# Performance work log

Measured on AMD Instinct MI355X. Metric: run time of the kernel, lower is better.

## Reference

```python
import jax, jax.numpy as jnp
import numpy as np

B, N, M = 4, 1024, 100
NB = 25
NTYPE = 2
TYPES = (1, 8)
FEAT = NB * NTYPE  # 50
H = 100
PI = 3.1415926
RMIN, RMAX = 0.5, 6.0


def setup_inputs() -> dict:
    key = jax.random.key(0)
    ks = jax.random.split(key, 12)
    type_map = jnp.array(TYPES)
    Imagetype = type_map[jax.random.randint(ks[0], (B, N), 0, NTYPE)]
    neighbor_list = jax.random.randint(ks[1], (B, N, M), 0, N + 1)
    rij = jax.random.uniform(ks[2], (B, N, M), minval=0.5, maxval=7.0)
    d = jax.random.normal(ks[3], (B, N, M, 3))
    d = d / jnp.linalg.norm(d, axis=-1, keepdims=True)
    ImagedR = jnp.concatenate([rij[..., None], d * rij[..., None]], axis=-1).astype(jnp.float32)

    def w(k, i, o):
        return (jax.random.normal(k, (NTYPE, i, o)) / np.sqrt(i + o)).astype(jnp.float32)

    def b(k, o):
        return jax.random.normal(k, (NTYPE, o)).astype(jnp.float32)

    return {"Imagetype": Imagetype, "neighbor_list": neighbor_list, "ImagedR": ImagedR,
            "W0": w(ks[4], FEAT, H), "b0": b(ks[5], H),
            "W1": w(ks[6], H, H), "b1": b(ks[7], H),
            "W2": w(ks[8], H, H), "b2": b(ks[9], H),
            "W3": w(ks[10], H, 1), "b3": b(ks[11], 1)}


def _net(x, W0, b0, W1, b1, W2, b2, W3, b3):
    # NET with network_size [50,100,100,100,1], tanh, resnet_dt=False
    h = jnp.tanh(x @ W0 + b0)
    x = h + jnp.concatenate([x, x], axis=-1)  # 50 -> 100 doubling skip
    h = jnp.tanh(x @ W1 + b1); x = h + x
    h = jnp.tanh(x @ W2 + b2); x = h + x
    return x @ W3 + b3


def _body2fun(Imagetype, neighbor_list, ImagedR):
    Bn, Nn, Mn = neighbor_list.shape
    rs = jnp.linspace(RMIN, RMAX, NB)  # [NB]
    r = ImagedR[..., 0]  # [B,N,M]
    rb = jnp.broadcast_to(r[..., None], (Bn, Nn, Mn, NB))

    def fc_fn(rt):
        env = jnp.exp(-(rt - rs) ** 2) * (0.5 * jnp.cos(PI * rt) + 0.5)
        return jnp.where((rt < RMAX) & (rt > 0), env, 0.0)

    # dfc = d(fc)/dr, elementwise, matching torch.autograd.grad with ones
    fc, dfc = jax.jvp(fc_fn, (rb,), (jnp.ones_like(rb),))

    # neighbor_type: 1-indexed lookup with 0 -> padding type 0
    padded = jnp.concatenate([jnp.zeros((Bn, 1), Imagetype.dtype), Imagetype], axis=1)
    nt = jnp.take_along_axis(padded, neighbor_list.reshape(Bn, -1), axis=1).reshape(Bn, Nn, Mn)

    dvec = jnp.where(r[..., None] != 0, ImagedR[..., 1:4] / r[..., None], 0.0)  # [B,N,M,3]

    feats, dfeats = [], []
    for t in TYPES:
        m = (nt == t)[..., None]  # [B,N,M,1]
        fct = jnp.where(m, fc, 0.0)
        dfct = jnp.where(m, dfc, 0.0)
        feats.append(fct.sum(axis=2))  # [B,N,NB]
        dfeats.append(dfct[..., None] * dvec[..., None, :])  # [B,N,M,NB,3]
    feat = jnp.concatenate(feats, axis=-1)  # [B,N,50]
    dfeat = jnp.concatenate(dfeats, axis=3)  # [B,N,M,50,3]
    return feat, dfeat


def reference(Imagetype, neighbor_list, ImagedR, W0, b0, W1, b1, W2, b2, W3, b3):
    Bn, Nn, Mn = neighbor_list.shape
    feat, dfeat = _body2fun(Imagetype, neighbor_list, ImagedR)

    type_arr = jnp.array(TYPES)
    mask = (Imagetype[None] == type_arr[:, None, None])[..., None]  # [T,B,N,1]

    def ei_fn(f):
        e = jax.vmap(_net, in_axes=(None, 0, 0, 0, 0, 0, 0, 0, 0))(
            f, W0, b0, W1, b1, W2, b2, W3, b3)  # [T,B,N,1]
        return jnp.sum(jnp.where(mask, e, 0.0), axis=0)  # [B,N,1]

    Ei = ei_fn(feat)
    Etot = jnp.sum(Ei, axis=1)  # [B,1]

    # dE/dfeat of total energy (grad_outputs = ones on Etot)
    dE = jax.grad(lambda f: jnp.sum(ei_fn(f)))(feat)  # [B,N,50]

    dE_Rid = jnp.einsum('bnf,bnmfc->bnmc', dE, dfeat)  # [B,N,M,3]
    Force = -dE_Rid.sum(axis=2)  # [B,N,3]

    # scatter-add of neighbor contributions: segment 0 is padding
    seg = jax.vmap(lambda v, i: jax.ops.segment_sum(v, i, num_segments=Nn + 1))(
        dE_Rid.reshape(Bn, -1, 3), neighbor_list.reshape(Bn, -1))  # [B,N+1,3]
    Force = Force + seg[:, 1:, :]
    return Etot, Ei, Force
```

## Files before the change

kernel.cpp:

```cpp
#include <hip/hip_runtime.h>

#define Bn   4
#define Nn   1024
#define Mn   100
#define NB   25
#define FEAT 50
#define PIc  3.1415926f
#define RSTEP (5.5f / 24.0f)

#define ATB  16
#define NATOMS (Bn * Nn)
#define ORDER_LEN (NATOMS + ATB)
#define MLP_BLOCKS (ORDER_LEN / ATB)
#define TYW  122880
#define PREP_BLKS 341

#define GPB  64
#define CPG  16
#define FTHREADS 512

typedef __attribute__((ext_vector_type(8))) short bf16x8;
typedef __attribute__((ext_vector_type(4))) float f32x4;

union U16x8 { unsigned short u[8]; bf16x8 v; uint4 q; };

__device__ __forceinline__ unsigned short f2bh(float x) {
    union { float f; unsigned u; } v; v.f = x;
    unsigned r = v.u + 0x7fffu + ((v.u >> 16) & 1u);
    return (unsigned short)(r >> 16);
}
__device__ __forceinline__ float bh2f(unsigned short h) {
    union { unsigned u; float f; } v; v.u = ((unsigned)h) << 16; return v.f;
}
__device__ __forceinline__ float fast_tanh(float x) {
    float ax = fabsf(x);
    float t  = __expf(-2.0f * ax);
    float r  = (1.0f - t) * __builtin_amdgcn_rcpf(1.0f + t);
    return copysignf(r, x);
}


__global__ __launch_bounds__(256) void stage1_kernel(
    const int* __restrict__ itype, const int* __restrict__ nlist,
    const float* __restrict__ dR,
    const float* __restrict__ W0, const float* __restrict__ W1,
    const float* __restrict__ W2,
    int* __restrict__ order, unsigned short* __restrict__ wsu,
    float* __restrict__ featp)
{
    const int blk = blockIdx.x;
    const int t = threadIdx.x;

    __shared__ float tile[64][65];
    __shared__ int scan[256];
    __shared__ float4 rc4[50];
    __shared__ float fpartial[64];

    if (blk < 20) {
        int ty = blk / 10, m = blk - ty * 10;
        int mat, jt, kt;
        if (m < 2)      { mat = 0; jt = m;            kt = 0; }
        else if (m < 6) { mat = 1; jt = (m - 2) >> 1; kt = (m - 2) & 1; }
        else            { mat = 2; jt = (m - 6) >> 1; kt = (m - 6) & 1; }
        const float* src = (mat == 0) ? W0 + ty * 5000
                          : (mat == 1) ? W1 + ty * 10000 : W2 + ty * 10000;
        const int Krows = (mat == 0) ? 50 : 100;
        const int Ck    = (mat == 0) ? 64 : 128;
        const int dH = ty * TYW + ((mat == 0) ? 0 : (mat == 1) ? 16384 : 49152);
        const int dL = dH + ((mat == 0) ? 8192 : 16384);
        const int j0 = jt * 64, k0 = kt * 64;
        const int rr0 = t >> 6, l = t & 63;
        #pragma unroll
        for (int i = 0; i < 16; ++i) {
            int rr = rr0 + 4 * i;
            int k = k0 + rr, j = j0 + l;
            tile[rr][l] = (k < Krows && j < 100) ? src[k * 100 + j] : 0.0f;
        }
        __syncthreads();
        #pragma unroll
        for (int i = 0; i < 16; ++i) {
            int jj = rr0 + 4 * i;
            float v = tile[l][jj];
            unsigned short h = f2bh(v);
            wsu[dH + (j0 + jj) * Ck + k0 + l] = h;
            wsu[dL + (j0 + jj) * Ck + k0 + l] = f2bh(v - bh2f(h));
        }
        return;
    }
    if (blk < 340) {
        int e = (blk - 20) * 256 + t;
        int ty = e / 40960;
        int r  = e - ty * 40960;
        float v = 0.0f; int dst;
        if (r < 16384) {
            int i = r >> 7, j = r & 127;
            if (i < 100 && j < 100) v = W2[ty * 10000 + i * 100 + j];
            dst = ty * TYW + 81920 + r;
        } else if (r < 32768) {
            int r2 = r - 16384; int i = r2 >> 7, j = r2 & 127;
            if (i < 100 && j < 100) v = W1[ty * 10000 + i * 100 + j];
            dst = ty * TYW + 98304 + r2;
        } else {
            int r2 = r - 32768; int f = r2 >> 7, j = r2 & 127;
            if (f < 50 && j < 100) v = W0[ty * 5000 + f * 100 + j];
            dst = ty * TYW + 114688 + r2;
        }
        wsu[dst] = f2bh(v);
        return;
    }
    if (blk == 340) {
        for (int i = t; i < ORDER_LEN; i += 256) order[i] = -1;
        int tyv[16]; int c0 = 0;
        #pragma unroll
        for (int k = 0; k < 16; ++k) {
            int tt = (itype[t * 16 + k] == 8) ? 1 : 0;
            tyv[k] = tt; c0 += 1 - tt;
        }
        scan[t] = c0;
        __syncthreads();
        for (int off = 1; off < 256; off <<= 1) {
            int v = scan[t];
            int add = (t >= off) ? scan[t - off] : 0;
            __syncthreads();
            scan[t] = v + add;
            __syncthreads();
        }
        int total0 = scan[255];
        int ex0 = scan[t] - c0;
        int ex1 = 16 * t - ex0;
        int pad0 = (total0 + (ATB - 1)) & ~(ATB - 1);
        int p0 = ex0, p1 = pad0 + ex1;
        #pragma unroll
        for (int k = 0; k < 16; ++k) {
            int idx = t * 16 + k;
            if (tyv[k] == 0) order[p0++] = idx; else order[p1++] = idx;
        }
        return;
    }

    const int atom = blk - PREP_BLKS;
    const int b = atom >> 10;

    if (t < Mn) {
        float4 qv = ((const float4*)dR)[(size_t)atom * Mn + t];
        float r = qv.x;
        int v = nlist[(size_t)atom * Mn + t];
        float cws = 0.0f;
        if (v > 0 && r > 0.0f && r < 6.0f) {
            float cw = 0.5f * __cosf(PIc * r) + 0.5f;
            cws = (itype[b * Nn + (v - 1)] == 8) ? -cw : cw;
        }
        ((float2*)rc4)[t] = make_float2(r, cws);
    }
    __syncthreads();

    float acc = 0.0f;
    if (t < 128) {
        const int w = t >> 6, l = t & 63;
        const int tt = l / NB;
        const float rk = 0.5f + (l - tt * NB) * RSTEP;
        #pragma unroll
        for (int i = 0; i < 25; ++i) {
            float4 pr = rc4[w * 25 + i];
            float d0 = pr.x - rk, d1 = pr.z - rk;
            float c0 = tt ? fmaxf(-pr.y, 0.0f) : fmaxf(pr.y, 0.0f);
            float c1 = tt ? fmaxf(-pr.w, 0.0f) : fmaxf(pr.w, 0.0f);
            acc += __expf(-d0 * d0) * c0 + __expf(-d1 * d1) * c1;
        }
        if (w == 1) fpartial[l] = acc;
    }
    __syncthreads();
    if (t < 64)
        featp[(size_t)atom * 64 + t] = (t < FEAT) ? (acc + fpartial[t]) : 0.0f;
}

#define ISSUE(RH, RL, OFFU, OFFL, RW, NKT, HASLO, COND)                       \
    if (COND) {                                                               \
        int jj_ = c + 16 * w;                                                 \
        _Pragma("unroll")                                                     \
        for (int kt = 0; kt < (NKT); ++kt) {                                  \
            int boff_ = jj_ * (RW) + kt * 32 + q * 8;                         \
            RH[kt] = *(const bf16x8*)(wb + (OFFU) + boff_);                   \
            if (HASLO) RL[kt] = *(const bf16x8*)(wb + (OFFL) + boff_);        \
        }                                                                     \
    }

#define GEMM_R(ABUF, RH, RL, NKT, HASLO)                                      \
    {                                                                         \
        acc = (f32x4){0,0,0,0}; accl = (f32x4){0,0,0,0};                      \
        _Pragma("unroll")                                                     \
        for (int kt = 0; kt < (NKT); ++kt) {                                  \
            int gk = kt * 4 + q;                                              \
            bf16x8 af = *(const bf16x8*)&aA[ABUF][(c << 7) | ((gk ^ (c & 7)) << 3)]; \
            acc = __builtin_amdgcn_mfma_f32_16x16x32_bf16(af, RH[kt], acc, 0, 0, 0); \
            if (HASLO) accl = __builtin_amdgcn_mfma_f32_16x16x32_bf16(af, RL[kt], accl, 0, 0, 0); \
        }                                                                     \
    }

#define WRACT(BUF, J, A, X)                                                   \
    aA[BUF][((A) << 7) | ((((J) >> 3) ^ ((A) & 7)) << 3) | ((J) & 7)] = f2bh(X)

__global__ __launch_bounds__(512) void mlp_kernel(
    const float* __restrict__ featp, const int* __restrict__ itype,
    const int* __restrict__ order, const unsigned short* __restrict__ wsu,
    const float* __restrict__ B0, const float* __restrict__ B1,
    const float* __restrict__ B2, const float* __restrict__ W3,
    const float* __restrict__ B3,
    float* __restrict__ Ei, float* __restrict__ dE)
{
    const int t = threadIdx.x;
    const int w = t >> 6;
    const int lane = t & 63;
    const int c = lane & 15, q = lane >> 4;

    __shared__ unsigned short aA[2][2048];
    __shared__ float fshf[16][52];
    __shared__ float dx1s[16][112];
    __shared__ float biasS[4][128];
    __shared__ float eip[8][16];
    __shared__ int aid[16];

    if (t < 16) aid[t] = order[blockIdx.x * ATB + t];
    __syncthreads();
    int first = -1;
    #pragma unroll
    for (int a = 0; a < ATB; ++a) { int v = aid[a]; if (first < 0 && v >= 0) first = v; }
    if (first < 0) return;
    const int ty = (itype[first] == 8) ? 1 : 0;
    const unsigned short* wb = wsu + (size_t)ty * TYW;

    bf16x8 bh0[4], bl0[4], bh1[4], bl1[4];
    f32x4 acc, accl;
    float xr[4], h0r[4], h1r[4], h2r[4], dxr[4];

    ISSUE(bh0, bl0, 0, 8192, 64, 2, 1, true);
    if (t < 128) {
        const int srow = t >> 3, sg = t & 7;
        int v = aid[srow];
        float4 fa = {0,0,0,0}, fb = {0,0,0,0};
        if (v >= 0) {
            const float4* fp = (const float4*)(featp + (size_t)v * 64 + sg * 8);
            fa = fp[0]; fb = fp[1];
        }
        U16x8 pk;
        pk.u[0]=f2bh(fa.x); pk.u[1]=f2bh(fa.y); pk.u[2]=f2bh(fa.z); pk.u[3]=f2bh(fa.w);
        pk.u[4]=f2bh(fb.x); pk.u[5]=f2bh(fb.y); pk.u[6]=f2bh(fb.z); pk.u[7]=f2bh(fb.w);
        *(uint4*)&aA[0][(srow << 7) | ((sg ^ (srow & 7)) << 3)] = pk.q;
        int cbase = sg * 8;
        if (cbase < 52) {
            float vals[8] = {fa.x,fa.y,fa.z,fa.w,fb.x,fb.y,fb.z,fb.w};
            #pragma unroll
            for (int j7 = 0; j7 < 8; ++j7)
                if (cbase + j7 < 52) fshf[srow][cbase + j7] = vals[j7];
        }
    }
    if (t < 512) {
        int row = t >> 7, col = t & 127;
        const float* s = (row == 0) ? B0 : (row == 1) ? B1 : (row == 2) ? B2 : W3;
        biasS[row][col] = (col < 100) ? s[ty * 100 + col] : 0.0f;
    }
    __syncthreads();

    ISSUE(bh1, bl1, 16384, 32768, 128, 4, 1, true);
    GEMM_R(0, bh0, bl0, 2, 1);
    {
        int j = c + 16 * w;
        float bj = biasS[0][j];
        #pragma unroll
        for (int r = 0; r < 4; ++r) {
            int a = q * 4 + r;
            float z = acc[r] + accl[r] + bj;
            float h = 0.f, x = 0.f;
            if (j < 100) { h = fast_tanh(z); x = h + fshf[a][(j < 50) ? j : j - 50]; }
            h0r[r] = h; xr[r] = x;
            WRACT(1, j, a, x);
        }
    }
    __syncthreads();

    ISSUE(bh0, bl0, 49152, 65536, 128, 4, 1, true);
    GEMM_R(1, bh1, bl1, 4, 1);
    {
        int j = c + 16 * w;
        float bj = biasS[1][j];
        #pragma unroll
        for (int r = 0; r < 4; ++r) {
            int a = q * 4 + r;
            float z = acc[r] + accl[r] + bj;
            float h = (j < 100) ? fast_tanh(z) : 0.f;
            float x = (j < 100) ? (h + xr[r]) : 0.f;
            h1r[r] = h; xr[r] = x;
            WRACT(0, j, a, x);
        }
    }
    __syncthreads();

    ISSUE(bh1, bl1, 81920, 0, 128, 4, 0, true);
    GEMM_R(0, bh0, bl0, 4, 1);
    {
        int j = c + 16 * w;
        float bj = biasS[2][j];
        float wv = biasS[3][j];
        float p4v[4];
        #pragma unroll
        for (int r = 0; r < 4; ++r) {
            float z = acc[r] + accl[r] + bj;
            float h = (j < 100) ? fast_tanh(z) : 0.f;
            h2r[r] = h;
            xr[r] = (j < 100) ? (h + xr[r]) : 0.f;
            p4v[r] = xr[r] * wv;
        }
        #pragma unroll
        for (int off = 1; off < 16; off <<= 1) {
            #pragma unroll
            for (int r = 0; r < 4; ++r) p4v[r] += __shfl_xor(p4v[r], off);
        }
        if (c == 0) {
            #pragma unroll
            for (int r = 0; r < 4; ++r) eip[w][q * 4 + r] = p4v[r];
        }
        #pragma unroll
        for (int r = 0; r < 4; ++r) {
            int a = q * 4 + r;
            float d = wv * (1.0f - h2r[r] * h2r[r]);
            WRACT(1, j, a, d);
        }
    }
    __syncthreads();
    if (t < 16) {
        int v = aid[t];
        if (v >= 0) {
            float e = B3[ty];
            #pragma unroll
            for (int ww = 0; ww < 8; ++ww) e += eip[ww][t];
            Ei[v] = e;
        }
    }

    ISSUE(bh0, bl0, 98304, 0, 128, 4, 0, true);
    GEMM_R(1, bh1, bl1, 4, 0);
    {
        int i = c + 16 * w;
        float w3i = biasS[3][i];
        #pragma unroll
        for (int r = 0; r < 4; ++r) {
            int a = q * 4 + r;
            float dx2 = acc[r] + w3i;
            dxr[r] = dx2;
            float d = dx2 * (1.0f - h1r[r] * h1r[r]);
            WRACT(0, i, a, d);
        }
    }
    __syncthreads();

    ISSUE(bh1, bl1, 114688, 0, 128, 4, 0, (w < 4));
    GEMM_R(0, bh0, bl0, 4, 0);
    {
        int i = c + 16 * w;
        #pragma unroll
        for (int r = 0; r < 4; ++r) {
            int a = q * 4 + r;
            float dx1 = dxr[r] + acc[r];
            if (i < 112) dx1s[a][i] = dx1;
            float d = dx1 * (1.0f - h0r[r] * h0r[r]);
            WRACT(1, i, a, d);
        }
    }
    __syncthreads();

    if (w < 4) {
        GEMM_R(1, bh1, bl1, 4, 0);
        int f = c + 16 * w;
        if (f < 50) {
            #pragma unroll
            for (int r = 0; r < 4; ++r) {
                int a = q * 4 + r;
                int v = aid[a];
                if (v >= 0) dE[(size_t)v * FEAT + f] = acc[r] + dx1s[a][f] + dx1s[a][f + 50];
            }
        }
    }
}

__global__ __launch_bounds__(FTHREADS) void force_kernel(
    const int* __restrict__ itype, const int* __restrict__ nlist,
    const float* __restrict__ dR, const float* __restrict__ dE,
    float* __restrict__ partial)
{
    const int blk = blockIdx.x;
    const int b = blk / GPB;
    const int g = blk - b * GPB;
    const int t = threadIdx.x;
    const int w = t >> 6, lane = t & 63;

    __shared__ float acc[(Nn + 1) * 3];
    __shared__ float desh[CPG][FEAT];

    for (int idx = t; idx < (Nn + 1) * 3; idx += FTHREADS) acc[idx] = 0.0f;
    for (int idx = t; idx < CPG * FEAT; idx += FTHREADS)
        ((float*)desh)[idx] = dE[((size_t)(b * Nn) + g * CPG) * FEAT + idx];
    __syncthreads();

    for (int cc = w; cc < CPG; cc += 8) {
        const int n = g * CPG + cc;
        const size_t pairbase = (size_t)(b * Nn + n) * Mn;

        const int m1 = lane + 64;
        float4 qv0 = ((const float4*)dR)[pairbase + lane];
        int    v0  = nlist[pairbase + lane];
        float4 qv1 = make_float4(0.f, 0.f, 0.f, 0.f);
        int    v1  = 0;
        if (m1 < Mn) {
            qv1 = ((const float4*)dR)[pairbase + m1];
            v1  = nlist[pairbase + m1];
        }

        float cfx = 0.f, cfy = 0.f, cfz = 0.f;
        #pragma unroll
        for (int mi = 0; mi < 2; ++mi) {
            float4 qv = mi ? qv1 : qv0;
            int v = mi ? v1 : v0;
            if (v > 0) {
                float r = qv.x;
                if (r > 0.0f && r < 6.0f) {
                    int tt = (itype[b * Nn + v - 1] == 8) ? 1 : 0;
                    float cw  = 0.5f * __cosf(PIc * r) + 0.5f;
                    float dcw = -0.5f * PIc * __sinf(PIc * r);
                    float s = 0.0f;
                    const float* de = &desh[cc][tt * NB];
                    #pragma unroll
                    for (int k = 0; k < NB; ++k) {
                        float d = r - (0.5f + k * RSTEP);
                        float e = __expf(-d * d);
                        s += de[k] * e * __builtin_fmaf(-2.0f * cw, d, dcw);
                    }
                    float inv = 1.0f / r;
                    float fx = s * qv.y * inv, fy = s * qv.z * inv, fz = s * qv.w * inv;
                    atomicAdd(&acc[v * 3 + 0], fx);
                    atomicAdd(&acc[v * 3 + 1], fy);
                    atomicAdd(&acc[v * 3 + 2], fz);
                    cfx += fx; cfy += fy; cfz += fz;
                }
            }
        }
        #pragma unroll
        for (int off = 32; off > 0; off >>= 1) {
            cfx += __shfl_xor(cfx, off);
            cfy += __shfl_xor(cfy, off);
            cfz += __shfl_xor(cfz, off);
        }
        if (lane == 0) {
            atomicAdd(&acc[(n + 1) * 3 + 0], -cfx);
            atomicAdd(&acc[(n + 1) * 3 + 1], -cfy);
            atomicAdd(&acc[(n + 1) * 3 + 2], -cfz);
        }
    }
    __syncthreads();

    float* pout = partial + (size_t)blk * ((Nn + 1) * 3);
    for (int idx = t; idx < (Nn + 1) * 3; idx += FTHREADS) pout[idx] = acc[idx];
}

__global__ __launch_bounds__(256) void freduce_kernel(
    const float* __restrict__ partial, const float* __restrict__ Ei,
    float* __restrict__ Force, float* __restrict__ Etot)
{
    if (blockIdx.x == 48) {
        const int t = threadIdx.x;
        __shared__ float red[256];
        for (int b = 0; b < Bn; ++b) {
            float s = 0.0f;
            for (int i = t; i < Nn; i += 256) s += Ei[b * Nn + i];
            red[t] = s;
            __syncthreads();
            for (int st = 128; st > 0; st >>= 1) {
                if (t < st) red[t] += red[t + st];
                __syncthreads();
            }
            if (t == 0) Etot[b] = red[0];
            __syncthreads();
        }
        return;
    }
    int idx = blockIdx.x * 256 + threadIdx.x;
    if (idx >= Bn * Nn * 3) return;
    int b = idx / (Nn * 3);
    int r = idx - b * (Nn * 3);
    int i = r / 3, ch = r - i * 3;
    float s = 0.0f;
    for (int g = 0; g < GPB; ++g)
        s += partial[((size_t)(b * GPB + g)) * ((Nn + 1) * 3) + (size_t)(i + 1) * 3 + ch];
    Force[idx] = s;
}

extern "C" void kernel_launch(void* const* d_in, const int* in_sizes, int n_in,
                              void* d_out, int out_size, void* d_ws, size_t ws_size,
                              hipStream_t stream)
{
    const int*   itype = (const int*)d_in[0];
    const int*   nlist = (const int*)d_in[1];
    const float* dR    = (const float*)d_in[2];
    const float* W0 = (const float*)d_in[3];  const float* B0 = (const float*)d_in[4];
    const float* W1 = (const float*)d_in[5];  const float* B1 = (const float*)d_in[6];
    const float* W2 = (const float*)d_in[7];  const float* B2 = (const float*)d_in[8];
    const float* W3 = (const float*)d_in[9];  const float* B3 = (const float*)d_in[10];

    float* out   = (float*)d_out;
    float* Etot  = out;
    float* Ei    = out + Bn;
    float* Force = out + Bn + Bn * Nn;

    float* featp   = (float*)d_ws;
    float* dEp     = featp + (size_t)NATOMS * 64;
    float* partial = dEp + (size_t)NATOMS * FEAT;
    int*   order   = (int*)(partial + (size_t)Bn * GPB * (Nn + 1) * 3);
    unsigned short* wsu = (unsigned short*)(order + ORDER_LEN);

    stage1_kernel <<<PREP_BLKS + NATOMS, 256, 0, stream>>>(itype, nlist, dR,
                                                           W0, W1, W2,
                                                           order, wsu, featp);
    mlp_kernel    <<<MLP_BLOCKS, 512, 0, stream>>>(featp, itype, order, wsu,
                                                   B0, B1, B2, W3, B3, Ei, dEp);
    force_kernel  <<<Bn * GPB, FTHREADS, 0, stream>>>(itype, nlist, dR, dEp, partial);
    freduce_kernel<<<49, 256, 0, stream>>>(partial, Ei, Force, Etot);
}
```

Measured before the change: 51.63 us.

## Fuse MLP and force kernels with per-batch type-sorted atom ordering

Merges the MLP kernel and the force scatter kernel into one kernel. Each block runs the MLP for 16 same-type atoms of a single batch, keeps dE in LDS, and accumulates force contributions into a per-block shared accumulator that is written out as a partial. The type ordering is now computed per batch so every block stays inside one batch, and Etot is accumulated with atomics instead of a separate reduction block. This removes one kernel launch and the global round trip of dE. The cost is a larger LDS footprint per block, 260 blocks instead of 257, and float atomics making Etot order-nondeterministic.

New measurement: 52.67 us. 1.02x slower.

```diff
diff --git a/kernel.cpp b/kernel.cpp
--- a/kernel.cpp
+++ b/kernel.cpp
@@ -10,14 +10,12 @@
 
 #define ATB  16
 #define NATOMS (Bn * Nn)
-#define ORDER_LEN (NATOMS + ATB)
-#define MLP_BLOCKS (ORDER_LEN / ATB)
+#define NGPB  65
+#define OBATCH (NGPB * ATB)
+#define MF_BLOCKS (Bn * NGPB)
 #define TYW  122880
 #define PREP_BLKS 341
-
-#define GPB  64
-#define CPG  16
-#define FTHREADS 512
+#define PSTRIDE ((Nn + 1) * 3)
 
 typedef __attribute__((ext_vector_type(8))) short bf16x8;
 typedef __attribute__((ext_vector_type(4))) float f32x4;
@@ -46,7 +44,7 @@
     const float* __restrict__ W0, const float* __restrict__ W1,
     const float* __restrict__ W2,
     int* __restrict__ order, unsigned short* __restrict__ wsu,
-    float* __restrict__ featp)
+    float* __restrict__ featp, float* __restrict__ Etot)
 {
     const int blk = blockIdx.x;
     const int t = threadIdx.x;
@@ -109,32 +107,38 @@
         return;
     }
     if (blk == 340) {
-        for (int i = t; i < ORDER_LEN; i += 256) order[i] = -1;
-        int tyv[16]; int c0 = 0;
-        #pragma unroll
-        for (int k = 0; k < 16; ++k) {
-            int tt = (itype[t * 16 + k] == 8) ? 1 : 0;
-            tyv[k] = tt; c0 += 1 - tt;
-        }
-        scan[t] = c0;
-        __syncthreads();
-        for (int off = 1; off < 256; off <<= 1) {
-            int v = scan[t];
-            int add = (t >= off) ? scan[t - off] : 0;
+        for (int i = t; i < Bn * OBATCH; i += 256) order[i] = -1;
+        __syncthreads();
+        for (int b = 0; b < Bn; ++b) {
+            int tyv[4]; int c0 = 0;
+            #pragma unroll
+            for (int k = 0; k < 4; ++k) {
+                int tt = (itype[b * Nn + t * 4 + k] == 8) ? 1 : 0;
+                tyv[k] = tt; c0 += 1 - tt;
+            }
+            scan[t] = c0;
             __syncthreads();
-            scan[t] = v + add;
+            for (int off = 1; off < 256; off <<= 1) {
+                int v = scan[t];
+                int add = (t >= off) ? scan[t - off] : 0;
+                __syncthreads();
+                scan[t] = v + add;
+                __syncthreads();
+            }
+            int total0 = scan[255];
+            int ex0 = scan[t] - c0;
+            int ex1 = 4 * t - ex0;
+            int pad0 = (total0 + (ATB - 1)) & ~(ATB - 1);
+            int p0 = ex0, p1 = pad0 + ex1;
+            #pragma unroll
+            for (int k = 0; k < 4; ++k) {
+                int n = t * 4 + k;
+                if (tyv[k] == 0) order[b * OBATCH + p0++] = n;
+                else             order[b * OBATCH + p1++] = n;
+            }
             __syncthreads();
         }
-        int total0 = scan[255];
-        int ex0 = scan[t] - c0;
-        int ex1 = 16 * t - ex0;
-        int pad0 = (total0 + (ATB - 1)) & ~(ATB - 1);
-        int p0 = ex0, p1 = pad0 + ex1;
-        #pragma unroll
-        for (int k = 0; k < 16; ++k) {
-            int idx = t * 16 + k;
-            if (tyv[k] == 0) order[p0++] = idx; else order[p1++] = idx;
-        }
+        if (t < Bn) Etot[t] = 0.0f;
         return;
     }
 
@@ -200,296 +204,279 @@
 #define WRACT(BUF, J, A, X)                                                   \
     aA[BUF][((A) << 7) | ((((J) >> 3) ^ ((A) & 7)) << 3) | ((J) & 7)] = f2bh(X)
 
-__global__ __launch_bounds__(512) void mlp_kernel(
+__global__ __launch_bounds__(512) void mlpforce_kernel(
     const float* __restrict__ featp, const int* __restrict__ itype,
+    const int* __restrict__ nlist, const float* __restrict__ dR,
     const int* __restrict__ order, const unsigned short* __restrict__ wsu,
     const float* __restrict__ B0, const float* __restrict__ B1,
     const float* __restrict__ B2, const float* __restrict__ W3,
     const float* __restrict__ B3,
-    float* __restrict__ Ei, float* __restrict__ dE)
+    float* __restrict__ Ei, float* __restrict__ Etot,
+    float* __restrict__ partial)
 {
     const int t = threadIdx.x;
     const int w = t >> 6;
     const int lane = t & 63;
     const int c = lane & 15, q = lane >> 4;
+    const int b = blockIdx.x / NGPB;
+    const int grp = blockIdx.x - b * NGPB;
 
     __shared__ unsigned short aA[2][2048];
     __shared__ float fshf[16][52];
     __shared__ float dx1s[16][112];
     __shared__ float biasS[4][128];
     __shared__ float eip[8][16];
+    __shared__ float eivals[16];
+    __shared__ float deLDS[16][52];
+    __shared__ float facc[PSTRIDE];
     __shared__ int aid[16];
 
-    if (t < 16) aid[t] = order[blockIdx.x * ATB + t];
+    for (int idx = t; idx < PSTRIDE; idx += 512) facc[idx] = 0.0f;
+    if (t < 16) aid[t] = order[b * OBATCH + grp * ATB + t];
     __syncthreads();
+
     int first = -1;
     #pragma unroll
     for (int a = 0; a < ATB; ++a) { int v = aid[a]; if (first < 0 && v >= 0) first = v; }
-    if (first < 0) return;
-    const int ty = (itype[first] == 8) ? 1 : 0;
-    const unsigned short* wb = wsu + (size_t)ty * TYW;
-
-    bf16x8 bh0[4], bl0[4], bh1[4], bl1[4];
-    f32x4 acc, accl;
-    float xr[4], h0r[4], h1r[4], h2r[4], dxr[4];
-
-    ISSUE(bh0, bl0, 0, 8192, 64, 2, 1, true);
-    if (t < 128) {
-        const int srow = t >> 3, sg = t & 7;
-        int v = aid[srow];
-        float4 fa = {0,0,0,0}, fb = {0,0,0,0};
-        if (v >= 0) {
-            const float4* fp = (const float4*)(featp + (size_t)v * 64 + sg * 8);
-            fa = fp[0]; fb = fp[1];
-        }
-        U16x8 pk;
-        pk.u[0]=f2bh(fa.x); pk.u[1]=f2bh(fa.y); pk.u[2]=f2bh(fa.z); pk.u[3]=f2bh(fa.w);
-        pk.u[4]=f2bh(fb.x); pk.u[5]=f2bh(fb.y); pk.u[6]=f2bh(fb.z); pk.u[7]=f2bh(fb.w);
-        *(uint4*)&aA[0][(srow << 7) | ((sg ^ (srow & 7)) << 3)] = pk.q;
-        int cbase = sg * 8;
-        if (cbase < 52) {
-            float vals[8] = {fa.x,fa.y,fa.z,fa.w,fb.x,fb.y,fb.z,fb.w};
-            #pragma unroll
-            for (int j7 = 0; j7 < 8; ++j7)
-                if (cbase + j7 < 52) fshf[srow][cbase + j7] = vals[j7];
-        }
-    }
-    if (t < 512) {
-        int row = t >> 7, col = t & 127;
-        const float* s = (row == 0) ? B0 : (row == 1) ? B1 : (row == 2) ? B2 : W3;
-        biasS[row][col] = (col < 100) ? s[ty * 100 + col] : 0.0f;
-    }
-    __syncthreads();
-
-    ISSUE(bh1, bl1, 16384, 32768, 128, 4, 1, true);
-    GEMM_R(0, bh0, bl0, 2, 1);
-    {
-        int j = c + 16 * w;
-        float bj = biasS[0][j];
-        #pragma unroll
-        for (int r = 0; r < 4; ++r) {
-            int a = q * 4 + r;
-            float z = acc[r] + accl[r] + bj;
-            float h = 0.f, x = 0.f;
-            if (j < 100) { h = fast_tanh(z); x = h + fshf[a][(j < 50) ? j : j - 50]; }
-            h0r[r] = h; xr[r] = x;
-            WRACT(1, j, a, x);
-        }
-    }
-    __syncthreads();
-
-    ISSUE(bh0, bl0, 49152, 65536, 128, 4, 1, true);
-    GEMM_R(1, bh1, bl1, 4, 1);
-    {
-        int j = c + 16 * w;
-        float bj = biasS[1][j];
-        #pragma unroll
-        for (int r = 0; r < 4; ++r) {
-            int a = q * 4 + r;
-            float z = acc[r] + accl[r] + bj;
-            float h = (j < 100) ? fast_tanh(z) : 0.f;
-            float x = (j < 100) ? (h + xr[r]) : 0.f;
-            h1r[r] = h; xr[r] = x;
-            WRACT(0, j, a, x);
-        }
-    }
-    __syncthreads();
-
-    ISSUE(bh1, bl1, 81920, 0, 128, 4, 0, true);
-    GEMM_R(0, bh0, bl0, 4, 1);
-    {
-        int j = c + 16 * w;
-        float bj = biasS[2][j];
-        float wv = biasS[3][j];
-        float p4v[4];
-        #pragma unroll
-        for (int r = 0; r < 4; ++r) {
-            float z = acc[r] + accl[r] + bj;
-            float h = (j < 100) ? fast_tanh(z) : 0.f;
-            h2r[r] = h;
-            xr[r] = (j < 100) ? (h + xr[r]) : 0.f;
-            p4v[r] = xr[r] * wv;
-        }
-        #pragma unroll
-        for (int off = 1; off < 16; off <<= 1) {
-            #pragma unroll
-            for (int r = 0; r < 4; ++r) p4v[r] += __shfl_xor(p4v[r], off);
-        }
-        if (c == 0) {
-            #pragma unroll
-            for (int r = 0; r < 4; ++r) eip[w][q * 4 + r] = p4v[r];
-        }
-        #pragma unroll
-        for (int r = 0; r < 4; ++r) {
-            int a = q * 4 + r;
-            float d = wv * (1.0f - h2r[r] * h2r[r]);
-            WRACT(1, j, a, d);
-        }
-    }
-    __syncthreads();
-    if (t < 16) {
-        int v = aid[t];
-        if (v >= 0) {
-            float e = B3[ty];
-            #pragma unroll
-            for (int ww = 0; ww < 8; ++ww) e += eip[ww][t];
-            Ei[v] = e;
-        }
-    }
-
-    ISSUE(bh0, bl0, 98304, 0, 128, 4, 0, true);
-    GEMM_R(1, bh1, bl1, 4, 0);
-    {
-        int i = c + 16 * w;
-        float w3i = biasS[3][i];
-        #pragma unroll
-        for (int r = 0; r < 4; ++r) {
-            int a = q * 4 + r;
-            float dx2 = acc[r] + w3i;
-            dxr[r] = dx2;
-            float d = dx2 * (1.0f - h1r[r] * h1r[r]);
-            WRACT(0, i, a, d);
-        }
-    }
-    __syncthreads();
-
-    ISSUE(bh1, bl1, 114688, 0, 128, 4, 0, (w < 4));
-    GEMM_R(0, bh0, bl0, 4, 0);
-    {
-        int i = c + 16 * w;
-        #pragma unroll
-        for (int r = 0; r < 4; ++r) {
-            int a = q * 4 + r;
-            float dx1 = dxr[r] + acc[r];
-            if (i < 112) dx1s[a][i] = dx1;
-            float d = dx1 * (1.0f - h0r[r] * h0r[r]);
-            WRACT(1, i, a, d);
-        }
-    }
-    __syncthreads();
-
-    if (w < 4) {
-        GEMM_R(1, bh1, bl1, 4, 0);
-        int f = c + 16 * w;
-        if (f < 50) {
+
+    if (first >= 0) {
+        const int ty = (itype[b * Nn + first] == 8) ? 1 : 0;
+        const unsigned short* wb = wsu + (size_t)ty * TYW;
+
+        bf16x8 bh0[4], bl0[4], bh1[4], bl1[4];
+        f32x4 acc, accl;
+        float xr[4], h0r[4], h1r[4], h2r[4], dxr[4];
+
+        ISSUE(bh0, bl0, 0, 8192, 64, 2, 1, true);
+        if (t < 128) {
+            const int srow = t >> 3, sg = t & 7;
+            int v = aid[srow];
+            float4 fa = {0,0,0,0}, fb = {0,0,0,0};
+            if (v >= 0) {
+                const float4* fp = (const float4*)(featp + ((size_t)(b * Nn + v)) * 64 + sg * 8);
+                fa = fp[0]; fb = fp[1];
+            }
+            U16x8 pk;
+            pk.u[0]=f2bh(fa.x); pk.u[1]=f2bh(fa.y); pk.u[2]=f2bh(fa.z); pk.u[3]=f2bh(fa.w);
+            pk.u[4]=f2bh(fb.x); pk.u[5]=f2bh(fb.y); pk.u[6]=f2bh(fb.z); pk.u[7]=f2bh(fb.w);
+            *(uint4*)&aA[0][(srow << 7) | ((sg ^ (srow & 7)) << 3)] = pk.q;
+            int cbase = sg * 8;
+            if (cbase < 52) {
+                float vals[8] = {fa.x,fa.y,fa.z,fa.w,fb.x,fb.y,fb.z,fb.w};
+                #pragma unroll
+                for (int j7 = 0; j7 < 8; ++j7)
+                    if (cbase + j7 < 52) fshf[srow][cbase + j7] = vals[j7];
+            }
+        }
+        {
+            int row = t >> 7, col = t & 127;
+            const float* s = (row == 0) ? B0 : (row == 1) ? B1 : (row == 2) ? B2 : W3;
+            biasS[row][col] = (col < 100) ? s[ty * 100 + col] : 0.0f;
+        }
+        __syncthreads();
+
+        ISSUE(bh1, bl1, 16384, 32768, 128, 4, 1, true);
+        GEMM_R(0, bh0, bl0, 2, 1);
+        {
+            int j = c + 16 * w;
+            float bj = biasS[0][j];
             #pragma unroll
             for (int r = 0; r < 4; ++r) {
                 int a = q * 4 + r;
-                int v = aid[a];
-                if (v >= 0) dE[(size_t)v * FEAT + f] = acc[r] + dx1s[a][f] + dx1s[a][f + 50];
-            }
-        }
-    }
-}
-
-__global__ __launch_bounds__(FTHREADS) void force_kernel(
-    const int* __restrict__ itype, const int* __restrict__ nlist,
-    const float* __restrict__ dR, const float* __restrict__ dE,
-    float* __restrict__ partial)
+                float z = acc[r] + accl[r] + bj;
+                float h = 0.f, x = 0.f;
+                if (j < 100) { h = fast_tanh(z); x = h + fshf[a][(j < 50) ? j : j - 50]; }
+                h0r[r] = h; xr[r] = x;
+                WRACT(1, j, a, x);
+            }
+        }
+        __syncthreads();
+
+        ISSUE(bh0, bl0, 49152, 65536, 128, 4, 1, true);
+        GEMM_R(1, bh1, bl1, 4, 1);
+        {
+            int j = c + 16 * w;
+            float bj = biasS[1][j];
+            #pragma unroll
+            for (int r = 0; r < 4; ++r) {
+                int a = q * 4 + r;
+                float z = acc[r] + accl[r] + bj;
+                float h = (j < 100) ? fast_tanh(z) : 0.f;
+                float x = (j < 100) ? (h + xr[r]) : 0.f;
+                h1r[r] = h; xr[r] = x;
+                WRACT(0, j, a, x);
+            }
+        }
+        __syncthreads();
+
+        ISSUE(bh1, bl1, 81920, 0, 128, 4, 0, true);
+        GEMM_R(0, bh0, bl0, 4, 1);
+        {
+            int j = c + 16 * w;
+            float bj = biasS[2][j];
+            float wv = biasS[3][j];
+            float p4v[4];
+            #pragma unroll
+            for (int r = 0; r < 4; ++r) {
+                float z = acc[r] + accl[r] + bj;
+                float h = (j < 100) ? fast_tanh(z) : 0.f;
+                h2r[r] = h;
+                xr[r] = (j < 100) ? (h + xr[r]) : 0.f;
+                p4v[r] = xr[r] * wv;
+            }
+            #pragma unroll
+            for (int off = 1; off < 16; off <<= 1) {
+                #pragma unroll
+                for (int r = 0; r < 4; ++r) p4v[r] += __shfl_xor(p4v[r], off);
+            }
+            if (c == 0) {
+                #pragma unroll
+                for (int r = 0; r < 4; ++r) eip[w][q * 4 + r] = p4v[r];
+            }
+            #pragma unroll
+            for (int r = 0; r < 4; ++r) {
+                int a = q * 4 + r;
+                float d = wv * (1.0f - h2r[r] * h2r[r]);
+                WRACT(1, j, a, d);
+            }
+        }
+        __syncthreads();
+        if (t < 16) {
+            int v = aid[t];
+            float e = 0.0f;
+            if (v >= 0) {
+                e = B3[ty];
+                #pragma unroll
+                for (int ww = 0; ww < 8; ++ww) e += eip[ww][t];
+                Ei[b * Nn + v] = e;
+            }
+            eivals[t] = e;
+        }
+
+        ISSUE(bh0, bl0, 98304, 0, 128, 4, 0, true);
+        GEMM_R(1, bh1, bl1, 4, 0);
+        {
+            int i = c + 16 * w;
+            float w3i = biasS[3][i];
+            #pragma unroll
+            for (int r = 0; r < 4; ++r) {
+                int a = q * 4 + r;
+                float dx2 = acc[r] + w3i;
+                dxr[r] = dx2;
+                float d = dx2 * (1.0f - h1r[r] * h1r[r]);
+                WRACT(0, i, a, d);
+            }
+        }
+        __syncthreads();
+
+        ISSUE(bh1, bl1, 114688, 0, 128, 4, 0, (w < 4));
+        GEMM_R(0, bh0, bl0, 4, 0);
+        {
+            int i = c + 16 * w;
+            #pragma unroll
+            for (int r = 0; r < 4; ++r) {
+                int a = q * 4 + r;
+                float dx1 = dxr[r] + acc[r];
+                if (i < 112) dx1s[a][i] = dx1;
+                float d = dx1 * (1.0f - h0r[r] * h0r[r]);
+                WRACT(1, i, a, d);
+            }
+        }
+        __syncthreads();
+
+        if (w < 4) {
+            GEMM_R(1, bh1, bl1, 4, 0);
+            int f = c + 16 * w;
+            if (f < 50) {
+                #pragma unroll
+                for (int r = 0; r < 4; ++r) {
+                    int a = q * 4 + r;
+                    deLDS[a][f] = acc[r] + dx1s[a][f] + dx1s[a][f + 50];
+                }
+            }
+        }
+        __syncthreads();
+
+        if (t == 0) {
+            float s = 0.0f;
+            #pragma unroll
+            for (int i = 0; i < 16; ++i) s += eivals[i];
+            atomicAdd(&Etot[b], s);
+        }
+        #pragma unroll
+        for (int ai = 0; ai < 2; ++ai) {
+            const int a = w * 2 + ai;
+            const int n = aid[a];
+            if (n >= 0) {
+                const size_t pairbase = (size_t)(b * Nn + n) * Mn;
+                const int m1 = lane + 64;
+                float4 qv0 = ((const float4*)dR)[pairbase + lane];
+                int    v0  = nlist[pairbase + lane];
+                float4 qv1 = make_float4(0.f, 0.f, 0.f, 0.f);
+                int    v1  = 0;
+                if (m1 < Mn) {
+                    qv1 = ((const float4*)dR)[pairbase + m1];
+                    v1  = nlist[pairbase + m1];
+                }
+                float cfx = 0.f, cfy = 0.f, cfz = 0.f;
+                #pragma unroll
+                for (int mi = 0; mi < 2; ++mi) {
+                    float4 qv = mi ? qv1 : qv0;
+                    int v = mi ? v1 : v0;
+                    if (v > 0) {
+                        float r = qv.x;
+                        if (r > 0.0f && r < 6.0f) {
+                            int tt = (itype[b * Nn + v - 1] == 8) ? 1 : 0;
+                            float cw  = 0.5f * __cosf(PIc * r) + 0.5f;
+                            float dcw = -0.5f * PIc * __sinf(PIc * r);
+                            float s = 0.0f;
+                            const float* de = &deLDS[a][tt * NB];
+                            #pragma unroll
+                            for (int k = 0; k < NB; ++k) {
+                                float d = r - (0.5f + k * RSTEP);
+                                float e = __expf(-d * d);
+                                s += de[k] * e * __builtin_fmaf(-2.0f * cw, d, dcw);
+                            }
+                            float inv = 1.0f / r;
+                            float fx = s * qv.y * inv, fy = s * qv.z * inv, fz = s * qv.w * inv;
+                            atomicAdd(&facc[v * 3 + 0], fx);
+                            atomicAdd(&facc[v * 3 + 1], fy);
+                            atomicAdd(&facc[v * 3 + 2], fz);
+                            cfx += fx; cfy += fy; cfz += fz;
+                        }
+                    }
+                }
+                #pragma unroll
+                for (int off = 32; off > 0; off >>= 1) {
+                    cfx += __shfl_xor(cfx, off);
+                    cfy += __shfl_xor(cfy, off);
+                    cfz += __shfl_xor(cfz, off);
+                }
+                if (lane == 0) {
+                    atomicAdd(&facc[(n + 1) * 3 + 0], -cfx);
+                    atomicAdd(&facc[(n + 1) * 3 + 1], -cfy);
+                    atomicAdd(&facc[(n + 1) * 3 + 2], -cfz);
+                }
+            }
+        }
+    }
+    __syncthreads();
+
+    float* pout = partial + (size_t)blockIdx.x * PSTRIDE;
+    for (int idx = t; idx < PSTRIDE; idx += 512) pout[idx] = facc[idx];
+}
+
+__global__ __launch_bounds__(256) void freduce_kernel(
+    const float* __restrict__ partial, float* __restrict__ Force)
 {
-    const int blk = blockIdx.x;
-    const int b = blk / GPB;
-    const int g = blk - b * GPB;
-    const int t = threadIdx.x;
-    const int w = t >> 6, lane = t & 63;
-
-    __shared__ float acc[(Nn + 1) * 3];
-    __shared__ float desh[CPG][FEAT];
-
-    for (int idx = t; idx < (Nn + 1) * 3; idx += FTHREADS) acc[idx] = 0.0f;
-    for (int idx = t; idx < CPG * FEAT; idx += FTHREADS)
-        ((float*)desh)[idx] = dE[((size_t)(b * Nn) + g * CPG) * FEAT + idx];
-    __syncthreads();
-
-    for (int cc = w; cc < CPG; cc += 8) {
-        const int n = g * CPG + cc;
-        const size_t pairbase = (size_t)(b * Nn + n) * Mn;
-
-        const int m1 = lane + 64;
-        float4 qv0 = ((const float4*)dR)[pairbase + lane];
-        int    v0  = nlist[pairbase + lane];
-        float4 qv1 = make_float4(0.f, 0.f, 0.f, 0.f);
-        int    v1  = 0;
-        if (m1 < Mn) {
-            qv1 = ((const float4*)dR)[pairbase + m1];
-            v1  = nlist[pairbase + m1];
-        }
-
-        float cfx = 0.f, cfy = 0.f, cfz = 0.f;
-        #pragma unroll
-        for (int mi = 0; mi < 2; ++mi) {
-            float4 qv = mi ? qv1 : qv0;
-            int v = mi ? v1 : v0;
-            if (v > 0) {
-                float r = qv.x;
-                if (r > 0.0f && r < 6.0f) {
-                    int tt = (itype[b * Nn + v - 1] == 8) ? 1 : 0;
-                    float cw  = 0.5f * __cosf(PIc * r) + 0.5f;
-                    float dcw = -0.5f * PIc * __sinf(PIc * r);
-                    float s = 0.0f;
-                    const float* de = &desh[cc][tt * NB];
-                    #pragma unroll
-                    for (int k = 0; k < NB; ++k) {
-                        float d = r - (0.5f + k * RSTEP);
-                        float e = __expf(-d * d);
-                        s += de[k] * e * __builtin_fmaf(-2.0f * cw, d, dcw);
-                    }
-                    float inv = 1.0f / r;
-                    float fx = s * qv.y * inv, fy = s * qv.z * inv, fz = s * qv.w * inv;
-                    atomicAdd(&acc[v * 3 + 0], fx);
-                    atomicAdd(&acc[v * 3 + 1], fy);
-                    atomicAdd(&acc[v * 3 + 2], fz);
-                    cfx += fx; cfy += fy; cfz += fz;
-                }
-            }
-        }
-        #pragma unroll
-        for (int off = 32; off > 0; off >>= 1) {
-            cfx += __shfl_xor(cfx, off);
-            cfy += __shfl_xor(cfy, off);
-            cfz += __shfl_xor(cfz, off);
-        }
-        if (lane == 0) {
-            atomicAdd(&acc[(n + 1) * 3 + 0], -cfx);
-            atomicAdd(&acc[(n + 1) * 3 + 1], -cfy);
-            atomicAdd(&acc[(n + 1) * 3 + 2], -cfz);
-        }
-    }
-    __syncthreads();
-
-    float* pout = partial + (size_t)blk * ((Nn + 1) * 3);
-    for (int idx = t; idx < (Nn + 1) * 3; idx += FTHREADS) pout[idx] = acc[idx];
-}
-
-__global__ __launch_bounds__(256) void freduce_kernel(
-    const float* __restrict__ partial, const float* __restrict__ Ei,
-    float* __restrict__ Force, float* __restrict__ Etot)
-{
-    if (blockIdx.x == 48) {
-        const int t = threadIdx.x;
-        __shared__ float red[256];
-        for (int b = 0; b < Bn; ++b) {
-            float s = 0.0f;
-            for (int i = t; i < Nn; i += 256) s += Ei[b * Nn + i];
-            red[t] = s;
-            __syncthreads();
-            for (int st = 128; st > 0; st >>= 1) {
-                if (t < st) red[t] += red[t + st];
-                __syncthreads();
-            }
-            if (t == 0) Etot[b] = red[0];
-            __syncthreads();
-        }
-        return;
-    }
     int idx = blockIdx.x * 256 + threadIdx.x;
     if (idx >= Bn * Nn * 3) return;
     int b = idx / (Nn * 3);
     int r = idx - b * (Nn * 3);
     int i = r / 3, ch = r - i * 3;
     float s = 0.0f;
-    for (int g = 0; g < GPB; ++g)
-        s += partial[((size_t)(b * GPB + g)) * ((Nn + 1) * 3) + (size_t)(i + 1) * 3 + ch];
+    for (int g = 0; g < NGPB; ++g)
+        s += partial[((size_t)(b * NGPB + g)) * PSTRIDE + (size_t)(i + 1) * 3 + ch];
     Force[idx] = s;
 }
 
@@ -511,16 +498,16 @@
     float* Force = out + Bn + Bn * Nn;
 
     float* featp   = (float*)d_ws;
-    float* dEp     = featp + (size_t)NATOMS * 64;
-    float* partial = dEp + (size_t)NATOMS * FEAT;
-    int*   order   = (int*)(partial + (size_t)Bn * GPB * (Nn + 1) * 3);
-    unsigned short* wsu = (unsigned short*)(order + ORDER_LEN);
-
-    stage1_kernel <<<PREP_BLKS + NATOMS, 256, 0, stream>>>(itype, nlist, dR,
-                                                           W0, W1, W2,
-                                                           order, wsu, featp);
-    mlp_kernel    <<<MLP_BLOCKS, 512, 0, stream>>>(featp, itype, order, wsu,
-                                                   B0, B1, B2, W3, B3, Ei, dEp);
-    force_kernel  <<<Bn * GPB, FTHREADS, 0, stream>>>(itype, nlist, dR, dEp, partial);
-    freduce_kernel<<<49, 256, 0, stream>>>(partial, Ei, Force, Etot);
-}
+    float* partial = featp + (size_t)NATOMS * 64;
+    int*   order   = (int*)(partial + (size_t)MF_BLOCKS * PSTRIDE);
+    unsigned short* wsu = (unsigned short*)(order + Bn * OBATCH);
+
+    stage1_kernel  <<<PREP_BLKS + NATOMS, 256, 0, stream>>>(itype, nlist, dR,
+                                                            W0, W1, W2,
+                                                            order, wsu, featp, Etot);
+    mlpforce_kernel<<<MF_BLOCKS, 512, 0, stream>>>(featp, itype, nlist, dR,
+                                                   order, wsu,
+                                                   B0, B1, B2, W3, B3,
+                                                   Ei, Etot, partial);
+    freduce_kernel <<<(Bn * Nn * 3 + 255) / 256, 256, 0, stream>>>(partial, Force);
+}
```
